# Kernel optimization log

Measured on AMD Instinct MI355X. Metric: run time of the kernel, lower is better.

The kernel has to match this reference:

```python
import jax, jax.numpy as jnp
import numpy as np

SCALE_FACTOR = 8.0  # sqrt(head_dim=64)

def setup_inputs() -> dict:
    key = jax.random.key(0)
    kq, kk, kv = jax.random.split(key, 3)
    BH, S, D = 64, 2048, 64  # batch*heads, seq_len, head_dim
    q = jax.random.normal(kq, (BH, S, D), dtype=jnp.float32)
    k = jax.random.normal(kk, (BH, S, D), dtype=jnp.float32)
    v = jax.random.normal(kv, (BH, S, D), dtype=jnp.float32)
    return {"q": q, "k": k, "v": v}

def reference(q, k, v):
    # qk = q @ k^T, scaled, softmax over keys, (dropout p=0 == identity), @ v
    scores = jnp.einsum("bqd,bkd->bqk", q, k) / SCALE_FACTOR  # [BH, S, S]
    attn = jax.nn.softmax(scores, axis=-1)
    out = jnp.einsum("bqk,bkd->bqd", attn, v)  # [BH, S, D]
    return out
```

## Files before the change

kernel.cpp:

```cpp
#include <hip/hip_runtime.h>
#include <hip/hip_bf16.h>


typedef __attribute__((ext_vector_type(8))) short short8;
typedef __attribute__((ext_vector_type(4))) short short4v;
typedef __attribute__((ext_vector_type(4))) float float4v;

#define S_LEN 2048
#define D_DIM 64
#define BH_N  64
#define LOG2E 1.4426950408889634f
#define CLF   (0.125f * LOG2E)

__device__ __forceinline__ unsigned int fpack2_fast(float a, float b) {
    unsigned int ua = __builtin_bit_cast(unsigned int, a) + 0x8000u;
    unsigned int ub = __builtin_bit_cast(unsigned int, b) + 0x8000u;
    return __builtin_amdgcn_perm(ub, ua, 0x07060302);
}
__device__ __forceinline__ unsigned int fpack2_trunc(float a, float b) {
    return __builtin_amdgcn_perm(__builtin_bit_cast(unsigned int, b),
                                 __builtin_bit_cast(unsigned int, a),
                                 0x07060302);
}
__device__ __forceinline__ void load16_lds(const unsigned short* g, unsigned short* l) {
    __builtin_amdgcn_global_load_lds(
        (const __attribute__((address_space(1))) unsigned int*)g,
        (__attribute__((address_space(3))) unsigned int*)l,
        16, 0, 0);
}

__global__ void __launch_bounds__(256) prep(const float* __restrict__ k,
                                            const float* __restrict__ v,
                                            unsigned short* __restrict__ kbf,
                                            unsigned short* __restrict__ vt) {
    __shared__ unsigned short T[64 * 66];
    const int b = blockIdx.x;
    const int t = threadIdx.x;
    if (b & 1) {
        const int kb = b >> 1;
        const size_t i = ((size_t)kb * 256 + t) * 16;
        #pragma unroll
        for (int j = 0; j < 2; ++j) {
            const float4 a0 = *(const float4*)(k + i + j * 8);
            const float4 a1 = *(const float4*)(k + i + j * 8 + 4);
            uint4 o;
            o.x = fpack2_fast(a0.x, a0.y); o.y = fpack2_fast(a0.z, a0.w);
            o.z = fpack2_fast(a1.x, a1.y); o.w = fpack2_fast(a1.z, a1.w);
            *(uint4*)(kbf + i + j * 8) = o;
        }
        return;
    }
    const int idx = b >> 1;
    const int kt = idx & 31, bh = idx >> 5;
    const float* Vg = v + ((size_t)bh * S_LEN + kt * 64) * D_DIM;
    #pragma unroll
    for (int it = 0; it < 4; ++it) {
        const int row = it * 16 + (t >> 4);
        const int col = (t & 15) * 4;
        const float4 f = *(const float4*)(Vg + row * 64 + col);
        unsigned int* p = (unsigned int*)&T[row * 66 + col];
        p[0] = fpack2_fast(f.x, f.y);
        p[1] = fpack2_fast(f.z, f.w);
    }
    __syncthreads();
    const int d  = t >> 2;
    const int cg = t & 3;
    unsigned int w8[8];
    #pragma unroll
    for (int cc = 0; cc < 2; ++cc) {
        const int c   = cg * 2 + cc;
        const int kb0 = (c >> 2) * 32 + (c & 3) * 4;
        w8[cc*4+0] = __builtin_amdgcn_perm(T[(kb0+ 1)*66+d], T[(kb0+ 0)*66+d], 0x05040100);
        w8[cc*4+1] = __builtin_amdgcn_perm(T[(kb0+ 3)*66+d], T[(kb0+ 2)*66+d], 0x05040100);
        w8[cc*4+2] = __builtin_amdgcn_perm(T[(kb0+17)*66+d], T[(kb0+16)*66+d], 0x05040100);
        w8[cc*4+3] = __builtin_amdgcn_perm(T[(kb0+19)*66+d], T[(kb0+18)*66+d], 0x05040100);
    }
    unsigned short* outp = vt + ((size_t)bh * 64 + d) * S_LEN + kt * 64 + cg * 16;
    uint4 o0; o0.x = w8[0]; o0.y = w8[1]; o0.z = w8[2]; o0.w = w8[3];
    uint4 o1; o1.x = w8[4]; o1.y = w8[5]; o1.z = w8[6]; o1.w = w8[7];
    *(uint4*)(outp)     = o0;
    *(uint4*)(outp + 8) = o1;
}

__global__ void __launch_bounds__(256, 4) attn_fwd7(
        const float* __restrict__ q, const unsigned short* __restrict__ kbf,
        const unsigned short* __restrict__ vt, float* __restrict__ out) {
    __shared__ __align__(16) unsigned short Klds[2][64 * 64];
    __shared__ __align__(16) unsigned short Vlds[2][64 * 64];

    const int tid  = threadIdx.x;
    const int lane = tid & 63;
    const int wave = tid >> 6;
    const int l16  = lane & 15;
    const int quad = lane >> 4;
    const int rsw  = l16 & 7;

    const int bh    = blockIdx.y;
    const int qbase = blockIdx.x * 128;

    const unsigned short* Kb = kbf + (size_t)bh * S_LEN * D_DIM;
    const unsigned short* Vb = vt  + (size_t)bh * D_DIM * S_LEN;

    short8 qf[2][2];
    #pragma unroll
    for (int s = 0; s < 2; ++s) {
        const int qg = qbase + s * 64 + wave * 16 + l16;
        const float* Qr = q + ((size_t)bh * S_LEN + qg) * D_DIM;
        #pragma unroll
        for (int h = 0; h < 2; ++h) {
            const float4 a = *(const float4*)(Qr + h * 32 + quad * 8);
            const float4 b = *(const float4*)(Qr + h * 32 + quad * 8 + 4);
            uint4 w;
            w.x = fpack2_fast(a.x * CLF, a.y * CLF);
            w.y = fpack2_fast(a.z * CLF, a.w * CLF);
            w.z = fpack2_fast(b.x * CLF, b.y * CLF);
            w.w = fpack2_fast(b.z * CLF, b.w * CLF);
            qf[s][h] = __builtin_bit_cast(short8, w);
        }
    }

    const int srow0  = wave * 16 + (lane >> 3);
    const int schunk = (lane & 7) ^ (lane >> 3);
    const int dsoff  = wave * 1024 + lane * 8;
    const int p0     = (quad ^ rsw) * 8;

    float4v acc[2][4];
    #pragma unroll
    for (int s = 0; s < 2; ++s)
        #pragma unroll
        for (int dt = 0; dt < 4; ++dt) acc[s][dt] = (float4v){0.f, 0.f, 0.f, 0.f};
    float l_acc[2] = {0.f, 0.f};

    auto stage = [&](int kt, int buf) {
        #pragma unroll
        for (int ss = 0; ss < 2; ++ss) {
            const int row = srow0 + ss * 8;
            load16_lds(Kb + ((size_t)(kt * 64 + row)) * 64 + schunk * 8,
                       &Klds[buf][dsoff + ss * 512]);
            load16_lds(Vb + (size_t)row * S_LEN + kt * 64 + schunk * 8,
                       &Vlds[buf][dsoff + ss * 512]);
        }
    };

    auto tile = [&](int buf) {
        float4v st[2][4];
        #pragma unroll
        for (int ks = 0; ks < 4; ++ks) {
            const unsigned short* kr = &Klds[buf][(ks * 16 + l16) * 64];
            const short8 kf0 = *(const short8*)(kr + p0);
            const short8 kf1 = *(const short8*)(kr + (p0 ^ 32));
            #pragma unroll
            for (int s = 0; s < 2; ++s) {
                float4v z = (float4v){0.f, 0.f, 0.f, 0.f};
                z = __builtin_amdgcn_mfma_f32_16x16x32_bf16(kf0, qf[s][0], z, 0, 0, 0);
                z = __builtin_amdgcn_mfma_f32_16x16x32_bf16(kf1, qf[s][1], z, 0, 0, 0);
                st[s][ks] = z;
            }
        }
        short8 pf8[2][2];
        #pragma unroll
        for (int s = 0; s < 2; ++s) {
            #pragma unroll
            for (int w = 0; w < 2; ++w) {
                const float e0 = __builtin_amdgcn_exp2f(st[s][2*w][0]);
                const float e1 = __builtin_amdgcn_exp2f(st[s][2*w][1]);
                const float e2 = __builtin_amdgcn_exp2f(st[s][2*w][2]);
                const float e3 = __builtin_amdgcn_exp2f(st[s][2*w][3]);
                const float f0 = __builtin_amdgcn_exp2f(st[s][2*w+1][0]);
                const float f1 = __builtin_amdgcn_exp2f(st[s][2*w+1][1]);
                const float f2 = __builtin_amdgcn_exp2f(st[s][2*w+1][2]);
                const float f3 = __builtin_amdgcn_exp2f(st[s][2*w+1][3]);
                l_acc[s] += ((e0 + e1) + (e2 + e3)) + ((f0 + f1) + (f2 + f3));
                uint4 u;
                u.x = fpack2_trunc(e0, e1); u.y = fpack2_trunc(e2, e3);
                u.z = fpack2_trunc(f0, f1); u.w = fpack2_trunc(f2, f3);
                pf8[s][w] = __builtin_bit_cast(short8, u);
            }
        }
        #pragma unroll
        for (int dt = 0; dt < 4; ++dt) {
            const unsigned short* vrow = &Vlds[buf][(dt * 16 + l16) * 64];
            const short8 vf0 = *(const short8*)(vrow + p0);
            const short8 vf1 = *(const short8*)(vrow + (p0 ^ 32));
            #pragma unroll
            for (int s = 0; s < 2; ++s) {
                acc[s][dt] = __builtin_amdgcn_mfma_f32_16x16x32_bf16(vf0, pf8[s][0], acc[s][dt], 0, 0, 0);
                acc[s][dt] = __builtin_amdgcn_mfma_f32_16x16x32_bf16(vf1, pf8[s][1], acc[s][dt], 0, 0, 0);
            }
        }
    };

    stage(0, 0);
    #pragma unroll 1
    for (int kt = 0; kt < S_LEN / 64; kt += 2) {
        __syncthreads();
        stage(kt + 1, 1);
        tile(0);
        __syncthreads();
        if (kt + 2 < S_LEN / 64) stage(kt + 2, 0);
        tile(1);
    }

    #pragma unroll
    for (int s = 0; s < 2; ++s) {
        float l = l_acc[s];
        l += __shfl_xor(l, 16, 64);
        l += __shfl_xor(l, 32, 64);
        const float inv = 1.0f / l;
        const int qg = qbase + s * 64 + wave * 16 + l16;
        float* Or = out + ((size_t)bh * S_LEN + qg) * D_DIM;
        #pragma unroll
        for (int dt = 0; dt < 4; ++dt) {
            float4 o;
            o.x = acc[s][dt][0] * inv; o.y = acc[s][dt][1] * inv;
            o.z = acc[s][dt][2] * inv; o.w = acc[s][dt][3] * inv;
            *(float4*)(Or + dt * 16 + quad * 4) = o;
        }
    }
}

#define KSTRIDE 72
__global__ void __launch_bounds__(256) attn_fwd(
        const float* __restrict__ q, const float* __restrict__ k,
        const float* __restrict__ v, float* __restrict__ out) {
    __shared__ __align__(16) unsigned short Klds[64 * KSTRIDE];
    __shared__ __align__(16) unsigned short Vlds[64 * KSTRIDE];
    const int tid  = threadIdx.x;
    const int lane = tid & 63;
    const int wave = tid >> 6;
    const int l16  = lane & 15;
    const int quad = lane >> 4;
    const int bh    = blockIdx.y;
    const int qg    = blockIdx.x * 64 + wave * 16 + l16;
    const float* Qr = q + ((size_t)bh * S_LEN + qg) * D_DIM;
    const float* Kb = k + (size_t)bh * S_LEN * D_DIM;
    const float* Vb = v + (size_t)bh * S_LEN * D_DIM;
    short8 qf[2];
    #pragma unroll
    for (int h = 0; h < 2; ++h) {
        const float4 a = *(const float4*)(Qr + h * 32 + quad * 8);
        const float4 b = *(const float4*)(Qr + h * 32 + quad * 8 + 4);
        uint4 w;
        w.x = fpack2_fast(a.x * CLF, a.y * CLF);
        w.y = fpack2_fast(a.z * CLF, a.w * CLF);
        w.z = fpack2_fast(b.x * CLF, b.y * CLF);
        w.w = fpack2_fast(b.z * CLF, b.w * CLF);
        qf[h] = __builtin_bit_cast(short8, w);
    }
    float4v acc[4];
    #pragma unroll
    for (int dt = 0; dt < 4; ++dt) acc[dt] = (float4v){0.f, 0.f, 0.f, 0.f};
    float l_acc = 0.f;
    for (int kt = 0; kt < S_LEN / 64; ++kt) {
        __syncthreads();
        {
            const float* Kg = Kb + (size_t)kt * 64 * D_DIM;
            #pragma unroll
            for (int i = 0; i < 4; ++i) {
                const int idx = tid + i * 256;
                const int row = idx >> 4;
                const int col = (idx & 15) << 2;
                const float4 f = *(const float4*)(Kg + row * 64 + col);
                uint2 w; w.x = fpack2_fast(f.x, f.y); w.y = fpack2_fast(f.z, f.w);
                *(uint2*)(&Klds[row * KSTRIDE + col]) = w;
            }
        }
        {
            const float* Vg = Vb + (size_t)kt * 64 * D_DIM;
            #pragma unroll
            for (int it = 0; it < 2; ++it) {
                const int rp   = (tid & 15) + (it << 4);
                const int cg   = tid >> 4;
                const int row0 = rp * 2;
                const int col  = cg * 4;
                const float4 a = *(const float4*)(Vg + row0 * 64 + col);
                const float4 b = *(const float4*)(Vg + (row0 + 1) * 64 + col);
                *(unsigned int*)(&Vlds[(col + 0) * KSTRIDE + row0]) = fpack2_fast(a.x, b.x);
                *(unsigned int*)(&Vlds[(col + 1) * KSTRIDE + row0]) = fpack2_fast(a.y, b.y);
                *(unsigned int*)(&Vlds[(col + 2) * KSTRIDE + row0]) = fpack2_fast(a.z, b.z);
                *(unsigned int*)(&Vlds[(col + 3) * KSTRIDE + row0]) = fpack2_fast(a.w, b.w);
            }
        }
        __syncthreads();
        float4v st[4];
        #pragma unroll
        for (int ks = 0; ks < 4; ++ks) {
            const unsigned short* kr = &Klds[(ks * 16 + l16) * KSTRIDE + quad * 8];
            const short8 kf0 = *(const short8*)(kr);
            const short8 kf1 = *(const short8*)(kr + 32);
            float4v z = (float4v){0.f, 0.f, 0.f, 0.f};
            z = __builtin_amdgcn_mfma_f32_16x16x32_bf16(kf0, qf[0], z, 0, 0, 0);
            z = __builtin_amdgcn_mfma_f32_16x16x32_bf16(kf1, qf[1], z, 0, 0, 0);
            st[ks] = z;
        }
        short4v pf[4];
        #pragma unroll
        for (int ks = 0; ks < 4; ++ks) {
            const float p0 = __builtin_amdgcn_exp2f(st[ks][0]);
            const float p1 = __builtin_amdgcn_exp2f(st[ks][1]);
            const float p2 = __builtin_amdgcn_exp2f(st[ks][2]);
            const float p3 = __builtin_amdgcn_exp2f(st[ks][3]);
            l_acc += (p0 + p1) + (p2 + p3);
            uint2 u; u.x = fpack2_trunc(p0, p1); u.y = fpack2_trunc(p2, p3);
            pf[ks] = __builtin_bit_cast(short4v, u);
        }
        #pragma unroll
        for (int dt = 0; dt < 4; ++dt) {
            const unsigned short* vr = &Vlds[(dt * 16 + l16) * KSTRIDE + quad * 4];
            #pragma unroll
            for (int ks = 0; ks < 4; ++ks) {
                const short4v vf = *(const short4v*)(vr + ks * 16);
                acc[dt] = __builtin_amdgcn_mfma_f32_16x16x16bf16_1k(vf, pf[ks], acc[dt], 0, 0, 0);
            }
        }
    }
    float l = l_acc;
    l += __shfl_xor(l, 16, 64);
    l += __shfl_xor(l, 32, 64);
    const float inv = 1.0f / l;
    float* Or = out + ((size_t)bh * S_LEN + qg) * D_DIM;
    #pragma unroll
    for (int dt = 0; dt < 4; ++dt) {
        float4 o;
        o.x = acc[dt][0] * inv; o.y = acc[dt][1] * inv;
        o.z = acc[dt][2] * inv; o.w = acc[dt][3] * inv;
        *(float4*)(Or + dt * 16 + quad * 4) = o;
    }
}

extern "C" void kernel_launch(void* const* d_in, const int* in_sizes, int n_in,
                              void* d_out, int out_size, void* d_ws, size_t ws_size,
                              hipStream_t stream) {
    const float* q = (const float*)d_in[0];
    const float* k = (const float*)d_in[1];
    const float* v = (const float*)d_in[2];
    float* out = (float*)d_out;
    const size_t need = (size_t)2 * BH_N * S_LEN * D_DIM * sizeof(unsigned short);
    if (ws_size >= need) {
        unsigned short* kbf = (unsigned short*)d_ws;
        unsigned short* vtp = kbf + (size_t)BH_N * S_LEN * D_DIM;
        prep<<<dim3(4096), 256, 0, stream>>>(k, v, kbf, vtp);
        attn_fwd7<<<dim3(S_LEN / 128, BH_N), 256, 0, stream>>>(q, kbf, vtp, out);
    } else {
        attn_fwd<<<dim3(S_LEN / 64, BH_N), 256, 0, stream>>>(q, k, v, out);
    }
}
```

Before: 200.5 us.

## Use two waves per block with 64 query rows per wave

Each block now runs 2 waves instead of 4, and each wave handles 64 query rows (4 sub-tiles of 16) instead of 32. K and V fragments read from LDS are reused across four query sub-tiles, which halves LDS reads per MFMA. Each thread now does twice as many staging loads. In exchange, register pressure rises because of the doubled accumulators and cached K fragments. Fewer waves per block, with launch bounds of 2 per SIMD hint, may also reduce the latency hiding available around barriers.

```diff
diff --git a/kernel.cpp b/kernel.cpp
--- a/kernel.cpp
+++ b/kernel.cpp
@@ -82,7 +82,7 @@
     *(uint4*)(outp + 8) = o1;
 }
 
-__global__ void __launch_bounds__(256, 4) attn_fwd7(
+__global__ void __launch_bounds__(128, 2) attn_fwd9(
         const float* __restrict__ q, const unsigned short* __restrict__ kbf,
         const unsigned short* __restrict__ vt, float* __restrict__ out) {
     __shared__ __align__(16) unsigned short Klds[2][64 * 64];
@@ -101,10 +101,10 @@
     const unsigned short* Kb = kbf + (size_t)bh * S_LEN * D_DIM;
     const unsigned short* Vb = vt  + (size_t)bh * D_DIM * S_LEN;
 
-    short8 qf[2][2];
-    #pragma unroll
-    for (int s = 0; s < 2; ++s) {
-        const int qg = qbase + s * 64 + wave * 16 + l16;
+    short8 qf[4][2];
+    #pragma unroll
+    for (int s = 0; s < 4; ++s) {
+        const int qg = qbase + wave * 64 + s * 16 + l16;
         const float* Qr = q + ((size_t)bh * S_LEN + qg) * D_DIM;
         #pragma unroll
         for (int h = 0; h < 2; ++h) {
@@ -119,21 +119,21 @@
         }
     }
 
-    const int srow0  = wave * 16 + (lane >> 3);
+    const int srow0  = wave * 32 + (lane >> 3);
     const int schunk = (lane & 7) ^ (lane >> 3);
-    const int dsoff  = wave * 1024 + lane * 8;
+    const int dsoff  = wave * 2048 + lane * 8;
     const int p0     = (quad ^ rsw) * 8;
 
-    float4v acc[2][4];
-    #pragma unroll
-    for (int s = 0; s < 2; ++s)
+    float4v acc[4][4];
+    #pragma unroll
+    for (int s = 0; s < 4; ++s)
         #pragma unroll
         for (int dt = 0; dt < 4; ++dt) acc[s][dt] = (float4v){0.f, 0.f, 0.f, 0.f};
-    float l_acc[2] = {0.f, 0.f};
+    float l_acc[4] = {0.f, 0.f, 0.f, 0.f};
 
     auto stage = [&](int kt, int buf) {
         #pragma unroll
-        for (int ss = 0; ss < 2; ++ss) {
+        for (int ss = 0; ss < 4; ++ss) {
             const int row = srow0 + ss * 8;
             load16_lds(Kb + ((size_t)(kt * 64 + row)) * 64 + schunk * 8,
                        &Klds[buf][dsoff + ss * 512]);
@@ -143,38 +143,39 @@
     };
 
     auto tile = [&](int buf) {
-        float4v st[2][4];
+        short8 kf[4][2];
         #pragma unroll
         for (int ks = 0; ks < 4; ++ks) {
             const unsigned short* kr = &Klds[buf][(ks * 16 + l16) * 64];
-            const short8 kf0 = *(const short8*)(kr + p0);
-            const short8 kf1 = *(const short8*)(kr + (p0 ^ 32));
-            #pragma unroll
-            for (int s = 0; s < 2; ++s) {
+            kf[ks][0] = *(const short8*)(kr + p0);
+            kf[ks][1] = *(const short8*)(kr + (p0 ^ 32));
+        }
+        short8 pf[4][2];
+        #pragma unroll
+        for (int s = 0; s < 4; ++s) {
+            float4v st[4];
+            #pragma unroll
+            for (int ks = 0; ks < 4; ++ks) {
                 float4v z = (float4v){0.f, 0.f, 0.f, 0.f};
-                z = __builtin_amdgcn_mfma_f32_16x16x32_bf16(kf0, qf[s][0], z, 0, 0, 0);
-                z = __builtin_amdgcn_mfma_f32_16x16x32_bf16(kf1, qf[s][1], z, 0, 0, 0);
-                st[s][ks] = z;
-            }
-        }
-        short8 pf8[2][2];
-        #pragma unroll
-        for (int s = 0; s < 2; ++s) {
+                z = __builtin_amdgcn_mfma_f32_16x16x32_bf16(kf[ks][0], qf[s][0], z, 0, 0, 0);
+                z = __builtin_amdgcn_mfma_f32_16x16x32_bf16(kf[ks][1], qf[s][1], z, 0, 0, 0);
+                st[ks] = z;
+            }
             #pragma unroll
             for (int w = 0; w < 2; ++w) {
-                const float e0 = __builtin_amdgcn_exp2f(st[s][2*w][0]);
-                const float e1 = __builtin_amdgcn_exp2f(st[s][2*w][1]);
-                const float e2 = __builtin_amdgcn_exp2f(st[s][2*w][2]);
-                const float e3 = __builtin_amdgcn_exp2f(st[s][2*w][3]);
-                const float f0 = __builtin_amdgcn_exp2f(st[s][2*w+1][0]);
-                const float f1 = __builtin_amdgcn_exp2f(st[s][2*w+1][1]);
-                const float f2 = __builtin_amdgcn_exp2f(st[s][2*w+1][2]);
-                const float f3 = __builtin_amdgcn_exp2f(st[s][2*w+1][3]);
+                const float e0 = __builtin_amdgcn_exp2f(st[2*w][0]);
+                const float e1 = __builtin_amdgcn_exp2f(st[2*w][1]);
+                const float e2 = __builtin_amdgcn_exp2f(st[2*w][2]);
+                const float e3 = __builtin_amdgcn_exp2f(st[2*w][3]);
+                const float f0 = __builtin_amdgcn_exp2f(st[2*w+1][0]);
+                const float f1 = __builtin_amdgcn_exp2f(st[2*w+1][1]);
+                const float f2 = __builtin_amdgcn_exp2f(st[2*w+1][2]);
+                const float f3 = __builtin_amdgcn_exp2f(st[2*w+1][3]);
                 l_acc[s] += ((e0 + e1) + (e2 + e3)) + ((f0 + f1) + (f2 + f3));
                 uint4 u;
                 u.x = fpack2_trunc(e0, e1); u.y = fpack2_trunc(e2, e3);
                 u.z = fpack2_trunc(f0, f1); u.w = fpack2_trunc(f2, f3);
-                pf8[s][w] = __builtin_bit_cast(short8, u);
+                pf[s][w] = __builtin_bit_cast(short8, u);
             }
         }
         #pragma unroll
@@ -183,9 +184,9 @@
             const short8 vf0 = *(const short8*)(vrow + p0);
             const short8 vf1 = *(const short8*)(vrow + (p0 ^ 32));
             #pragma unroll
-            for (int s = 0; s < 2; ++s) {
-                acc[s][dt] = __builtin_amdgcn_mfma_f32_16x16x32_bf16(vf0, pf8[s][0], acc[s][dt], 0, 0, 0);
-                acc[s][dt] = __builtin_amdgcn_mfma_f32_16x16x32_bf16(vf1, pf8[s][1], acc[s][dt], 0, 0, 0);
+            for (int s = 0; s < 4; ++s) {
+                acc[s][dt] = __builtin_amdgcn_mfma_f32_16x16x32_bf16(vf0, pf[s][0], acc[s][dt], 0, 0, 0);
+                acc[s][dt] = __builtin_amdgcn_mfma_f32_16x16x32_bf16(vf1, pf[s][1], acc[s][dt], 0, 0, 0);
             }
         }
     };
@@ -202,12 +203,12 @@
     }
 
     #pragma unroll
-    for (int s = 0; s < 2; ++s) {
+    for (int s = 0; s < 4; ++s) {
         float l = l_acc[s];
         l += __shfl_xor(l, 16, 64);
         l += __shfl_xor(l, 32, 64);
         const float inv = 1.0f / l;
-        const int qg = qbase + s * 64 + wave * 16 + l16;
+        const int qg = qbase + wave * 64 + s * 16 + l16;
         float* Or = out + ((size_t)bh * S_LEN + qg) * D_DIM;
         #pragma unroll
         for (int dt = 0; dt < 4; ++dt) {
@@ -340,7 +341,7 @@
         unsigned short* kbf = (unsigned short*)d_ws;
         unsigned short* vtp = kbf + (size_t)BH_N * S_LEN * D_DIM;
         prep<<<dim3(4096), 256, 0, stream>>>(k, v, kbf, vtp);
-        attn_fwd7<<<dim3(S_LEN / 128, BH_N), 256, 0, stream>>>(q, kbf, vtp, out);
+        attn_fwd9<<<dim3(S_LEN / 128, BH_N), 128, 0, stream>>>(q, kbf, vtp, out);
     } else {
         attn_fwd<<<dim3(S_LEN / 64, BH_N), 256, 0, stream>>>(q, k, v, out);
     }
```

Measured after the change: 203.3 us. Within noise of the previous version (+1.4%).
